# Performance work log

Measured on AMD Instinct MI355X. Metric: run time of the kernel, lower is better.

Reference implementation:

```python
import jax, jax.numpy as jnp
import numpy as np

D_MODEL = 512
T_MAX = 1000.0


def setup_inputs() -> dict:
    key = jax.random.key(0)
    t = jax.random.uniform(key, (524288,), dtype=jnp.float32) * T_MAX
    return {"t": t}


def reference(t) -> jnp.ndarray:
    # i = 0..d_model-1; freq_i = 10000 ** (2*i / d_model)
    i = jnp.arange(D_MODEL, dtype=jnp.float32)  # [D]
    inv_freq = jnp.exp(-(2.0 * i / D_MODEL) * jnp.log(jnp.float32(10000.0)))  # [D]
    arg = t[..., None] * inv_freq  # [B, D]
    even = (jnp.arange(D_MODEL) % 2) == 0  # sin at even i, cos at odd i
    return jnp.where(even, jnp.sin(arg), jnp.cos(arg))
```

## Files before the change

kernel.cpp:

```cpp
#include <hip/hip_runtime.h>
#include <math.h>


#define D_MODEL 512

typedef float f32x4 __attribute__((ext_vector_type(4)));

__device__ __forceinline__ float sin_rev(float r) {
    return __builtin_amdgcn_sinf(__builtin_amdgcn_fractf(r));
}
__device__ __forceinline__ float cos_rev(float r) {
    return __builtin_amdgcn_cosf(__builtin_amdgcn_fractf(r));
}

__global__ __launch_bounds__(256) void time_embed_kernel(
    const float* __restrict__ t, f32x4* __restrict__ out, int n_rows) {
    const int g = blockIdx.x * 256 + threadIdx.x;
    const int c = g & 63;
    const int w = g >> 6;

    const float LOG2_10000_OVER_256 = 0.051904345232615426f;
    const float INV_2PI = 0.15915494309189535f;

    float fa[4], fb[4];
#pragma unroll
    for (int j = 0; j < 4; ++j) {
        fa[j] = __builtin_amdgcn_exp2f(-(float)(4 * c + j) * LOG2_10000_OVER_256) * INV_2PI;
        fb[j] = __builtin_amdgcn_exp2f(-(float)(4 * c + 256 + j) * LOG2_10000_OVER_256) * INV_2PI;
    }

    const int row0 = w * 64;
    if (row0 >= n_rows) return;
    const float* tw = t + row0;
    f32x4* outw = out + (size_t)row0 * (D_MODEL / 4);

    f32x4 tq = *(const f32x4*)tw;
#pragma unroll 4
    for (int q = 0; q < 16; ++q) {
        const int qn = (q < 15) ? (q + 1) : q;
        const f32x4 tnext = *(const f32x4*)(tw + 4 * qn);

#pragma unroll
        for (int j = 0; j < 4; ++j) {
            const float tv = tq[j];
            f32x4 oa, ob;
            oa.x = sin_rev(tv * fa[0]);
            oa.y = cos_rev(tv * fa[1]);
            oa.z = sin_rev(tv * fa[2]);
            oa.w = cos_rev(tv * fa[3]);
            ob.x = sin_rev(tv * fb[0]);
            ob.y = cos_rev(tv * fb[1]);
            ob.z = sin_rev(tv * fb[2]);
            ob.w = cos_rev(tv * fb[3]);
            f32x4* rowp = outw + (size_t)(4 * q + j) * (D_MODEL / 4);
            rowp[c] = oa;
            rowp[64 + c] = ob;
        }
        tq = tnext;
    }
}

extern "C" void kernel_launch(void* const* d_in, const int* in_sizes, int n_in,
                              void* d_out, int out_size, void* d_ws, size_t ws_size,
                              hipStream_t stream) {
    const float* t = (const float*)d_in[0];
    f32x4* out = (f32x4*)d_out;
    const int n_rows = in_sizes[0];
    time_embed_kernel<<<dim3(2048), dim3(256), 0, stream>>>(t, out, n_rows);
}
```

Measured before the change: 201.7 us.

## Use persistent waves over contiguous row chunks with readlane broadcast of t

The grid shrinks from 2048 to 256 blocks, and each wave now handles a contiguous chunk of rows in 64-row segments. Instead of every lane loading the same four t values, each lane loads one t per segment and the value is broadcast with readlane. This cuts redundant loads and per-wave frequency setup, and keeps writes streaming through a long contiguous region. The cost is fewer waves in flight to hide store latency, and the code only covers all rows if n_rows divides evenly by 64 times the wave count.

```diff
diff --git a/kernel.cpp b/kernel.cpp
--- a/kernel.cpp
+++ b/kernel.cpp
@@ -16,8 +16,9 @@
 __global__ __launch_bounds__(256) void time_embed_kernel(
     const float* __restrict__ t, f32x4* __restrict__ out, int n_rows) {
     const int g = blockIdx.x * 256 + threadIdx.x;
-    const int c = g & 63;
+    const int lane = threadIdx.x & 63;
     const int w = g >> 6;
+    const int nw = (gridDim.x * 256) >> 6;
 
     const float LOG2_10000_OVER_256 = 0.051904345232615426f;
     const float INV_2PI = 0.15915494309189535f;
@@ -25,38 +26,43 @@
     float fa[4], fb[4];
 #pragma unroll
     for (int j = 0; j < 4; ++j) {
-        fa[j] = __builtin_amdgcn_exp2f(-(float)(4 * c + j) * LOG2_10000_OVER_256) * INV_2PI;
-        fb[j] = __builtin_amdgcn_exp2f(-(float)(4 * c + 256 + j) * LOG2_10000_OVER_256) * INV_2PI;
+        fa[j] = __builtin_amdgcn_exp2f(-(float)(4 * lane + j) * LOG2_10000_OVER_256) * INV_2PI;
+        fb[j] = __builtin_amdgcn_exp2f(-(float)(4 * lane + 256 + j) * LOG2_10000_OVER_256) * INV_2PI;
     }
 
-    const int row0 = w * 64;
+    const int rows_per_wave = n_rows / nw;
+    const int row0 = w * rows_per_wave;
     if (row0 >= n_rows) return;
     const float* tw = t + row0;
     f32x4* outw = out + (size_t)row0 * (D_MODEL / 4);
 
-    f32x4 tq = *(const f32x4*)tw;
-#pragma unroll 4
-    for (int q = 0; q < 16; ++q) {
-        const int qn = (q < 15) ? (q + 1) : q;
-        const f32x4 tnext = *(const f32x4*)(tw + 4 * qn);
+    const int nseg = rows_per_wave >> 6;
+    float tl = tw[lane];
+    for (int seg = 0; seg < nseg; ++seg) {
+        const int segn = (seg + 1 < nseg) ? (seg + 1) : seg;
+        const float tln = tw[segn * 64 + lane];
 
+        f32x4* sp = outw + (size_t)seg * 64 * (D_MODEL / 4);
+        for (int r8 = 0; r8 < 8; ++r8) {
 #pragma unroll
-        for (int j = 0; j < 4; ++j) {
-            const float tv = tq[j];
-            f32x4 oa, ob;
-            oa.x = sin_rev(tv * fa[0]);
-            oa.y = cos_rev(tv * fa[1]);
-            oa.z = sin_rev(tv * fa[2]);
-            oa.w = cos_rev(tv * fa[3]);
-            ob.x = sin_rev(tv * fb[0]);
-            ob.y = cos_rev(tv * fb[1]);
-            ob.z = sin_rev(tv * fb[2]);
-            ob.w = cos_rev(tv * fb[3]);
-            f32x4* rowp = outw + (size_t)(4 * q + j) * (D_MODEL / 4);
-            rowp[c] = oa;
-            rowp[64 + c] = ob;
+            for (int j = 0; j < 8; ++j) {
+                const float tv = __int_as_float(
+                    __builtin_amdgcn_readlane(__float_as_int(tl), r8 * 8 + j));
+                f32x4 oa, ob;
+                oa.x = sin_rev(tv * fa[0]);
+                oa.y = cos_rev(tv * fa[1]);
+                oa.z = sin_rev(tv * fa[2]);
+                oa.w = cos_rev(tv * fa[3]);
+                ob.x = sin_rev(tv * fb[0]);
+                ob.y = cos_rev(tv * fb[1]);
+                ob.z = sin_rev(tv * fb[2]);
+                ob.w = cos_rev(tv * fb[3]);
+                f32x4* rowp = sp + (size_t)(r8 * 8 + j) * (D_MODEL / 4);
+                rowp[lane] = oa;
+                rowp[64 + lane] = ob;
+            }
         }
-        tq = tnext;
+        tl = tln;
     }
 }
 
@@ -66,5 +72,5 @@
     const float* t = (const float*)d_in[0];
     f32x4* out = (f32x4*)d_out;
     const int n_rows = in_sizes[0];
-    time_embed_kernel<<<dim3(2048), dim3(256), 0, stream>>>(t, out, n_rows);
+    time_embed_kernel<<<dim3(256), dim3(256), 0, stream>>>(t, out, n_rows);
 }
```

Result: no change. 200.4 us (median of 2 runs) (-0.6%).
